# Performance work log

Hardware: AMD Instinct MI355X
Metric: run time of the kernel (lower is better)

The kernel has to match this reference:

```python
import jax, jax.numpy as jnp
import numpy as np

V = 25000
E = 100000
NODE_IN = 74
EDGE_IN = 12
OUT = 64
EHID = 128
NUM_STEPS = 6


def setup_inputs() -> dict:
    key = jax.random.key(0)
    ks = jax.random.split(key, 12)
    s = 0.05
    node_feats = jax.random.normal(ks[0], (V, NODE_IN), dtype=jnp.float32)
    edge_feats = jax.random.normal(ks[1], (E, EDGE_IN), dtype=jnp.float32)
    src = jax.random.randint(ks[2], (E,), 0, V)
    dst = jax.random.randint(ks[3], (E,), 0, V)
    # project_node_feats: Linear(node_in, out)
    Wp = jax.random.normal(ks[4], (NODE_IN, OUT), dtype=jnp.float32) * s
    bp = jnp.zeros((OUT,), dtype=jnp.float32)
    # edge network: Linear(edge_in, ehid) -> ReLU -> Linear(ehid, out*out)
    We1 = jax.random.normal(ks[5], (EDGE_IN, EHID), dtype=jnp.float32) * s
    be1 = jnp.zeros((EHID,), dtype=jnp.float32)
    We2 = jax.random.normal(ks[6], (EHID, OUT * OUT), dtype=jnp.float32) * s
    be2 = jnp.zeros((OUT * OUT,), dtype=jnp.float32)
    # NNConv output bias
    bias = jnp.zeros((OUT,), dtype=jnp.float32)
    return {
        "node_feats": node_feats, "edge_feats": edge_feats,
        "src": src, "dst": dst,
        "Wp": Wp, "bp": bp,
        "We1": We1, "be1": be1, "We2": We2, "be2": be2,
        "bias": bias,
    }


def reference(node_feats, edge_feats, src, dst, Wp, bp, We1, be1, We2, be2, bias):
    # project node features
    h = jax.nn.relu(node_feats @ Wp + bp)  # [V, OUT]
    # per-edge weight matrices (same every step -> hoist out of loop)
    ew = jax.nn.relu(edge_feats @ We1 + be1) @ We2 + be2  # [E, OUT*OUT]
    ew = ew.reshape(E, OUT, OUT)
    for _ in range(NUM_STEPS):
        # gather src node feats, batched matvec, scatter-sum to dst
        msg = jnp.einsum('ei,eio->eo', h[src], ew)  # [E, OUT]
        agg = jax.ops.segment_sum(msg, dst, num_segments=V)  # [V, OUT]
        h = jax.nn.relu(agg + bias)
    return h
```

## Files before the change

kernel.cpp:

```cpp
#include <hip/hip_runtime.h>
#include <hip/hip_bf16.h>

#define Vn 25000
#define En 100000
#define NODE_IN 74
#define EDGE_IN 12
#define OUTD 64
#define EHID 128
#define NUM_STEPS 6

#define HPAD 68

typedef __attribute__((ext_vector_type(8))) _Float16 half8;
typedef __attribute__((ext_vector_type(4))) float floatx4;

__global__ void proj_kernel(const float* __restrict__ node,
                            const float* __restrict__ Wp,
                            const float* __restrict__ bp,
                            float* __restrict__ h) {
  __shared__ float nf[NODE_IN];
  int v = blockIdx.x;
  int o = threadIdx.x;
  for (int i = o; i < NODE_IN; i += 64) nf[i] = node[(size_t)v * NODE_IN + i];
  __syncthreads();
  float acc = bp[o];
  for (int i = 0; i < NODE_IN; ++i) acc = fmaf(nf[i], Wp[i * OUTD + o], acc);
  h[(size_t)v * OUTD + o] = fmaxf(acc, 0.0f);
}

__global__ void edge_kernel(const float* __restrict__ ef,
                            const float* __restrict__ We1,
                            const float* __restrict__ be1,
                            _Float16* __restrict__ f) {
  __shared__ float es[EDGE_IN];
  int e = blockIdx.x;
  int k = threadIdx.x;
  if (k < EDGE_IN) es[k] = ef[(size_t)e * EDGE_IN + k];
  __syncthreads();
  float acc = be1[k];
  for (int j = 0; j < EDGE_IN; ++j) acc = fmaf(es[j], We1[j * EHID + k], acc);
  f[(size_t)e * EHID + k] = (_Float16)fmaxf(acc, 0.0f);
}

__global__ void w2r_kernel(const float* __restrict__ We2,
                           _Float16* __restrict__ w2s) {
  int g = blockIdx.x * 256 + threadIdx.x;
  int j = g & 7;
  int quad = (g >> 3) & 3;
  int l15 = (g >> 5) & 15;
  int c = (g >> 9) & 3;
  int step = g >> 11;
  int s = step & 3;
  int i = step >> 2;
  int k = s * 32 + quad * 8 + j;
  int col = i * 64 + c * 16 + l15;
  int eidx = g & 2047;
  int estore = eidx ^ (((eidx >> 6) & 3) << 3);
  w2s[((size_t)step << 11) | estore] = (_Float16)We2[(size_t)k * (OUTD * OUTD) + col];
}

#define GLOAD_LDS(gp, lp)                                                     \
  __builtin_amdgcn_global_load_lds(                                           \
      (const __attribute__((address_space(1))) void*)(gp),                    \
      (__attribute__((address_space(3))) void*)(lp), 16, 0, 0)

__global__ __launch_bounds__(256, 3) void msg_kernel(
    const float* __restrict__ h,
    const _Float16* __restrict__ f,
    const _Float16* __restrict__ w2s,
    const int* __restrict__ src,
    const int* __restrict__ dst,
    const float* __restrict__ be2,
    float* __restrict__ agg) {
  __shared__ __align__(16) float smem[12544];
  __shared__ int s_dst[64];

  const int tid = threadIdx.x;
  const int wv = tid >> 6;
  const int lane = tid & 63;
  const int quad = lane >> 4;
  const int l15 = lane & 15;
  const int e0 = blockIdx.x * 64;

  if (tid < 64) {
    int e = e0 + tid;
    s_dst[tid] = (e < En) ? dst[e] : -1;
  }
  {
    int e = tid & 63;
    int ib = tid >> 6;
    int eg = e0 + e;
    int sv = (eg < En) ? src[eg] : 0;
    const float4* hp = reinterpret_cast<const float4*>(h + (size_t)sv * OUTD + ib * 16);
    for (int c = 0; c < 4; ++c) {
      float4 val = hp[c];
      int i4 = ib * 16 + c * 4;
      smem[(i4 + 0) * HPAD + e] = val.x;
      smem[(i4 + 1) * HPAD + e] = val.y;
      smem[(i4 + 2) * HPAD + e] = val.z;
      smem[(i4 + 3) * HPAD + e] = val.w;
    }
  }
  __syncthreads();

  half8 afr[4][4];
#pragma unroll
  for (int t = 0; t < 4; ++t) {
    int e = e0 + t * 16 + l15;
    if (e >= En) e = En - 1;
    const _Float16* fr = f + (size_t)e * EHID + quad * 8;
#pragma unroll
    for (int s = 0; s < 4; ++s)
      afr[t][s] = *reinterpret_cast<const half8*>(fr + s * 32);
  }

  floatx4 acc[4][4];
  const floatx4 zero4 = (floatx4){0.f, 0.f, 0.f, 0.f};
#pragma unroll
  for (int t = 0; t < 4; ++t)
#pragma unroll
    for (int c = 0; c < 4; ++c) acc[t][c] = zero4;

  const int ibase = wv * 16;

  char* ring = (char*)smem + 4352 * 4 + wv * 8192;
  const char* w2b = (const char*)w2s;
  const int roff = l15 * 64 + ((quad ^ ((l15 >> 1) & 3)) << 4);
  const char* slot0p = ring + roff;
  const char* slot1p = ring + 4096 + roff;

#define STAGE(GS, SLOT)                                                       \
  {                                                                           \
    const char* gp_ = w2b + (size_t)(GS) * 4096 + lane * 16;                  \
    char* lp_ = ring + (SLOT) * 4096;                                         \
    GLOAD_LDS(gp_, lp_);                                                      \
    GLOAD_LDS(gp_ + 1024, lp_ + 1024);                                        \
    GLOAD_LDS(gp_ + 2048, lp_ + 2048);                                        \
    GLOAD_LDS(gp_ + 3072, lp_ + 3072);                                        \
  }

#define VM4 asm volatile("s_waitcnt vmcnt(4)" ::: "memory")
#define VM0 asm volatile("s_waitcnt vmcnt(0)" ::: "memory")
#define LGKM0 asm volatile("s_waitcnt lgkmcnt(0)" ::: "memory")

#define KSTEP(SS, SLOTP, SLOT, WAIT, DOSTAGE, IV)                             \
  {                                                                           \
    WAIT;                                                                     \
    half8 b0_ = *reinterpret_cast<const half8*>(SLOTP);                       \
    half8 b1_ = *reinterpret_cast<const half8*>(SLOTP + 1024);                \
    half8 b2_ = *reinterpret_cast<const half8*>(SLOTP + 2048);                \
    half8 b3_ = *reinterpret_cast<const half8*>(SLOTP + 3072);                \
    LGKM0;                                                                    \
    __builtin_amdgcn_sched_barrier(0);                                        \
    if (DOSTAGE) STAGE(((IV) << 2) + (SS) + 2, SLOT);                         \
    _Pragma("unroll") for (int t = 0; t < 4; ++t) {                           \
      half8 as = afr[t][SS] * hb[t];                                          \
      acc[t][0] = __builtin_amdgcn_mfma_f32_16x16x32_f16(as, b0_, acc[t][0], 0, 0, 0); \
      acc[t][1] = __builtin_amdgcn_mfma_f32_16x16x32_f16(as, b1_, acc[t][1], 0, 0, 0); \
      acc[t][2] = __builtin_amdgcn_mfma_f32_16x16x32_f16(as, b2_, acc[t][2], 0, 0, 0); \
      acc[t][3] = __builtin_amdgcn_mfma_f32_16x16x32_f16(as, b3_, acc[t][3], 0, 0, 0); \
    }                                                                         \
  }

#define BUILD_HB(IV)                                                          \
  half8 hb[4];                                                                \
  _Pragma("unroll") for (int t = 0; t < 4; ++t) {                             \
    _Float16 hf = (_Float16)smem[(IV) * HPAD + t * 16 + l15];                 \
    hb[t] = (half8){hf, hf, hf, hf, hf, hf, hf, hf};                          \
  }

  STAGE(ibase * 4, 0);
  STAGE(ibase * 4 + 1, 1);

  for (int ii = 0; ii < 15; ++ii) {
    int iv = ibase + ii;
    BUILD_HB(iv);
    KSTEP(0, slot0p, 0, VM4, 1, iv);
    KSTEP(1, slot1p, 1, VM4, 1, iv);
    KSTEP(2, slot0p, 0, VM4, 1, iv);
    KSTEP(3, slot1p, 1, VM4, 1, iv);
  }
  {
    int iv = ibase + 15;
    BUILD_HB(iv);
    KSTEP(0, slot0p, 0, VM4, 1, iv);
    KSTEP(1, slot1p, 1, VM4, 1, iv);
    KSTEP(2, slot0p, 0, VM4, 0, iv);
    KSTEP(3, slot1p, 1, VM0, 0, iv);
  }

  if (wv == 0) {
#pragma unroll
    for (int s = 0; s < 2; ++s) {
      half8 b2f[4];
#pragma unroll
      for (int c = 0; c < 4; ++c) {
        half8 v;
#pragma unroll
        for (int j = 0; j < 8; ++j)
          v[j] = (_Float16)be2[(s * 32 + quad * 8 + j) * 64 + c * 16 + l15];
        b2f[c] = v;
      }
#pragma unroll
      for (int t = 0; t < 4; ++t) {
        half8 ha;
#pragma unroll
        for (int j = 0; j < 8; ++j)
          ha[j] = (_Float16)smem[(s * 32 + quad * 8 + j) * HPAD + t * 16 + l15];
#pragma unroll
        for (int c = 0; c < 4; ++c)
          acc[t][c] = __builtin_amdgcn_mfma_f32_16x16x32_f16(ha, b2f[c], acc[t][c], 0, 0, 0);
      }
    }
  }

  floatx4* scv = reinterpret_cast<floatx4*>(smem);

#define ST1(TG)                                                           \
  _Pragma("unroll") for (int c = 0; c < 4; ++c)                           \
      scv[wv * 512 + (((TG) & 1) * 4 + c) * 64 + lane] = acc[TG][c];
#define LD1(TK)                                                           \
  _Pragma("unroll") for (int c = 0; c < 4; ++c)                           \
      acc[TK][c] += scv[(wv ^ 1) * 512 + (((TK) & 1) * 4 + c) * 64 + lane];
#define ST2(TG)                                                           \
  _Pragma("unroll") for (int c = 0; c < 4; ++c)                           \
      scv[wv * 512 + c * 64 + lane] = acc[TG][c];
#define LD2(TK)                                                           \
  _Pragma("unroll") for (int c = 0; c < 4; ++c)                           \
      acc[TK][c] += scv[(wv ^ 2) * 512 + c * 64 + lane];
#define SCAT(TF)                                                          \
  {                                                                       \
    int rb = (TF) * 16 + quad * 4;                                        \
    _Pragma("unroll") for (int c = 0; c < 4; ++c) {                       \
      int col = c * 16 + l15;                                             \
      _Pragma("unroll") for (int r = 0; r < 4; ++r) {                     \
        int d = s_dst[rb + r];                                            \
        if (d >= 0) atomicAdd(&agg[(size_t)d * OUTD + col], acc[TF][c][r]); \
      }                                                                   \
    }                                                                     \
  }

  __syncthreads();
  if ((wv & 1) == 0) { ST1(2); ST1(3); } else { ST1(0); ST1(1); }
  __syncthreads();
  if ((wv & 1) == 0) { LD1(0); LD1(1); } else { LD1(2); LD1(3); }
  __syncthreads();
  if (wv == 0) { ST2(1); } else if (wv == 1) { ST2(3); }
  else if (wv == 2) { ST2(0); } else { ST2(2); }
  __syncthreads();
  if (wv == 0) { LD2(0); SCAT(0); }
  else if (wv == 1) { LD2(2); SCAT(2); }
  else if (wv == 2) { LD2(1); SCAT(1); }
  else { LD2(3); SCAT(3); }
}

__global__ void update_kernel(float* __restrict__ agg,
                              const float* __restrict__ bias,
                              float* __restrict__ hout,
                              float* __restrict__ dout, int last) {
  int g = blockIdx.x * 256 + threadIdx.x;
  if (g >= Vn * OUTD) return;
  float v = agg[g];
  agg[g] = 0.0f;
  float r = fmaxf(v + bias[g & 63], 0.0f);
  hout[g] = r;
  if (last) dout[g] = r;
}

extern "C" void kernel_launch(void* const* d_in, const int* in_sizes, int n_in,
                              void* d_out, int out_size, void* d_ws, size_t ws_size,
                              hipStream_t stream) {
  const float* node = (const float*)d_in[0];
  const float* edge = (const float*)d_in[1];
  const int* src = (const int*)d_in[2];
  const int* dst = (const int*)d_in[3];
  const float* Wp   = (const float*)d_in[4];
  const float* bp   = (const float*)d_in[5];
  const float* We1  = (const float*)d_in[6];
  const float* be1  = (const float*)d_in[7];
  const float* We2  = (const float*)d_in[8];
  const float* be2  = (const float*)d_in[9];
  const float* bias = (const float*)d_in[10];
  float* out = (float*)d_out;

  char* ws = (char*)d_ws;
  float* agg = (float*)(ws);
  float* h_a = (float*)(ws + 6400000);
  float* h_b = (float*)(ws + 12800000);
  _Float16* f   = (_Float16*)(ws + 19200000);
  _Float16* w2s = (_Float16*)(ws + 44800000);

  hipMemsetAsync(agg, 0, (size_t)Vn * OUTD * sizeof(float), stream);
  proj_kernel<<<Vn, 64, 0, stream>>>(node, Wp, bp, h_a);
  edge_kernel<<<En, 128, 0, stream>>>(edge, We1, be1, f);
  w2r_kernel<<<(OUTD * OUTD * EHID) / 256, 256, 0, stream>>>(We2, w2s);

  float* hin = h_a;
  float* hout = h_b;
  for (int s = 0; s < NUM_STEPS; ++s) {
    msg_kernel<<<(En + 63) / 64, 256, 0, stream>>>(hin, f, w2s, src, dst, be2, agg);
    update_kernel<<<(Vn * OUTD + 255) / 256, 256, 0, stream>>>(
        agg, bias, hout, out, s == NUM_STEPS - 1);
    float* t = hin; hin = hout; hout = t;
  }
}
```

Before: 810.1 us.

## Software-pipeline LDS B-fragment reads with register double buffering in msg kernel

```diff
diff --git a/kernel.cpp b/kernel.cpp
--- a/kernel.cpp
+++ b/kernel.cpp
@@ -64,7 +64,7 @@
       (const __attribute__((address_space(1))) void*)(gp),                    \
       (__attribute__((address_space(3))) void*)(lp), 16, 0, 0)
 
-__global__ __launch_bounds__(256, 3) void msg_kernel(
+__global__ __launch_bounds__(256, 2) void msg_kernel(
     const float* __restrict__ h,
     const _Float16* __restrict__ f,
     const _Float16* __restrict__ w2s,
@@ -72,8 +72,10 @@
     const int* __restrict__ dst,
     const float* __restrict__ be2,
     float* __restrict__ agg) {
-  __shared__ __align__(16) float smem[12544];
+  __shared__ __align__(16) char smem_raw[41472];
   __shared__ int s_dst[64];
+
+  _Float16* h16 = (_Float16*)smem_raw;
 
   const int tid = threadIdx.x;
   const int wv = tid >> 6;
@@ -95,10 +97,10 @@
     for (int c = 0; c < 4; ++c) {
       float4 val = hp[c];
       int i4 = ib * 16 + c * 4;
-      smem[(i4 + 0) * HPAD + e] = val.x;
-      smem[(i4 + 1) * HPAD + e] = val.y;
-      smem[(i4 + 2) * HPAD + e] = val.z;
-      smem[(i4 + 3) * HPAD + e] = val.w;
+      h16[(i4 + 0) * HPAD + e] = (_Float16)val.x;
+      h16[(i4 + 1) * HPAD + e] = (_Float16)val.y;
+      h16[(i4 + 2) * HPAD + e] = (_Float16)val.z;
+      h16[(i4 + 3) * HPAD + e] = (_Float16)val.w;
     }
   }
   __syncthreads();
@@ -123,7 +125,7 @@
 
   const int ibase = wv * 16;
 
-  char* ring = (char*)smem + 4352 * 4 + wv * 8192;
+  char* ring = smem_raw + 8704 + wv * 8192;
   const char* w2b = (const char*)w2s;
   const int roff = l15 * 64 + ((quad ^ ((l15 >> 1) & 3)) << 4);
   const char* slot0p = ring + roff;
@@ -142,51 +144,64 @@
 #define VM4 asm volatile("s_waitcnt vmcnt(4)" ::: "memory")
 #define VM0 asm volatile("s_waitcnt vmcnt(0)" ::: "memory")
 #define LGKM0 asm volatile("s_waitcnt lgkmcnt(0)" ::: "memory")
-
-#define KSTEP(SS, SLOTP, SLOT, WAIT, DOSTAGE, IV)                             \
+#define LGKM4 asm volatile("s_waitcnt lgkmcnt(4)" ::: "memory")
+#define SB __builtin_amdgcn_sched_barrier(0)
+
+#define KSTEP(SS, BCUR, BNXT, STSLOT, GST, LW, VW, DO_STAGE, DO_READ, RDP)    \
   {                                                                           \
-    WAIT;                                                                     \
-    half8 b0_ = *reinterpret_cast<const half8*>(SLOTP);                       \
-    half8 b1_ = *reinterpret_cast<const half8*>(SLOTP + 1024);                \
-    half8 b2_ = *reinterpret_cast<const half8*>(SLOTP + 2048);                \
-    half8 b3_ = *reinterpret_cast<const half8*>(SLOTP + 3072);                \
-    LGKM0;                                                                    \
-    __builtin_amdgcn_sched_barrier(0);                                        \
-    if (DOSTAGE) STAGE(((IV) << 2) + (SS) + 2, SLOT);                         \
+    LW;                                                                       \
+    SB;                                                                       \
+    if (DO_STAGE) STAGE(GST, STSLOT);                                         \
+    VW;                                                                       \
+    if (DO_READ) {                                                            \
+      BNXT[0] = *reinterpret_cast<const half8*>(RDP);                         \
+      BNXT[1] = *reinterpret_cast<const half8*>(RDP + 1024);                  \
+      BNXT[2] = *reinterpret_cast<const half8*>(RDP + 2048);                  \
+      BNXT[3] = *reinterpret_cast<const half8*>(RDP + 3072);                  \
+    }                                                                         \
     _Pragma("unroll") for (int t = 0; t < 4; ++t) {                           \
       half8 as = afr[t][SS] * hb[t];                                          \
-      acc[t][0] = __builtin_amdgcn_mfma_f32_16x16x32_f16(as, b0_, acc[t][0], 0, 0, 0); \
-      acc[t][1] = __builtin_amdgcn_mfma_f32_16x16x32_f16(as, b1_, acc[t][1], 0, 0, 0); \
-      acc[t][2] = __builtin_amdgcn_mfma_f32_16x16x32_f16(as, b2_, acc[t][2], 0, 0, 0); \
-      acc[t][3] = __builtin_amdgcn_mfma_f32_16x16x32_f16(as, b3_, acc[t][3], 0, 0, 0); \
+      acc[t][0] = __builtin_amdgcn_mfma_f32_16x16x32_f16(as, BCUR[0], acc[t][0], 0, 0, 0); \
+      acc[t][1] = __builtin_amdgcn_mfma_f32_16x16x32_f16(as, BCUR[1], acc[t][1], 0, 0, 0); \
+      acc[t][2] = __builtin_amdgcn_mfma_f32_16x16x32_f16(as, BCUR[2], acc[t][2], 0, 0, 0); \
+      acc[t][3] = __builtin_amdgcn_mfma_f32_16x16x32_f16(as, BCUR[3], acc[t][3], 0, 0, 0); \
     }                                                                         \
+    SB;                                                                       \
   }
 
 #define BUILD_HB(IV)                                                          \
   half8 hb[4];                                                                \
   _Pragma("unroll") for (int t = 0; t < 4; ++t) {                             \
-    _Float16 hf = (_Float16)smem[(IV) * HPAD + t * 16 + l15];                 \
+    _Float16 hf = h16[(IV) * HPAD + t * 16 + l15];                            \
     hb[t] = (half8){hf, hf, hf, hf, hf, hf, hf, hf};                          \
   }
 
   STAGE(ibase * 4, 0);
   STAGE(ibase * 4 + 1, 1);
+  VM4;
+  half8 bE[4], bO[4];
+  bE[0] = *reinterpret_cast<const half8*>(slot0p);
+  bE[1] = *reinterpret_cast<const half8*>(slot0p + 1024);
+  bE[2] = *reinterpret_cast<const half8*>(slot0p + 2048);
+  bE[3] = *reinterpret_cast<const half8*>(slot0p + 3072);
 
   for (int ii = 0; ii < 15; ++ii) {
     int iv = ibase + ii;
+    int gs = iv * 4;
     BUILD_HB(iv);
-    KSTEP(0, slot0p, 0, VM4, 1, iv);
-    KSTEP(1, slot1p, 1, VM4, 1, iv);
-    KSTEP(2, slot0p, 0, VM4, 1, iv);
-    KSTEP(3, slot1p, 1, VM4, 1, iv);
+    KSTEP(0, bE, bO, 0, gs + 2, LGKM4, VM4, 1, 1, slot1p);
+    KSTEP(1, bO, bE, 1, gs + 3, LGKM0, VM4, 1, 1, slot0p);
+    KSTEP(2, bE, bO, 0, gs + 4, LGKM0, VM4, 1, 1, slot1p);
+    KSTEP(3, bO, bE, 1, gs + 5, LGKM0, VM4, 1, 1, slot0p);
   }
   {
     int iv = ibase + 15;
+    int gs = iv * 4;
     BUILD_HB(iv);
-    KSTEP(0, slot0p, 0, VM4, 1, iv);
-    KSTEP(1, slot1p, 1, VM4, 1, iv);
-    KSTEP(2, slot0p, 0, VM4, 0, iv);
-    KSTEP(3, slot1p, 1, VM0, 0, iv);
+    KSTEP(0, bE, bO, 0, gs + 2, LGKM4, VM4, 1, 1, slot1p);
+    KSTEP(1, bO, bE, 1, gs + 3, LGKM0, VM4, 1, 1, slot0p);
+    KSTEP(2, bE, bO, 0, 0, LGKM0, VM0, 0, 1, slot1p);
+    KSTEP(3, bO, bE, 1, 0, (void)0, (void)0, 0, 0, slot0p);
   }
 
   if (wv == 0) {
@@ -206,7 +221,7 @@
         half8 ha;
 #pragma unroll
         for (int j = 0; j < 8; ++j)
-          ha[j] = (_Float16)smem[(s * 32 + quad * 8 + j) * HPAD + t * 16 + l15];
+          ha[j] = h16[(s * 32 + quad * 8 + j) * HPAD + t * 16 + l15];
 #pragma unroll
         for (int c = 0; c < 4; ++c)
           acc[t][c] = __builtin_amdgcn_mfma_f32_16x16x32_f16(ha, b2f[c], acc[t][c], 0, 0, 0);
@@ -214,7 +229,7 @@
     }
   }
 
-  floatx4* scv = reinterpret_cast<floatx4*>(smem);
+  floatx4* scv = reinterpret_cast<floatx4*>(smem_raw);
 
 #define ST1(TG)                                                           \
   _Pragma("unroll") for (int c = 0; c < 4; ++c)                           \
```

Result: slower. 839.2 us (+3.6%).

## Run message kernel as single-wave blocks over full K, dropping cross-wave reduction

Applied to the files above, without the earlier changes.

```diff
diff --git a/kernel.cpp b/kernel.cpp
--- a/kernel.cpp
+++ b/kernel.cpp
@@ -8,8 +8,6 @@
 #define OUTD 64
 #define EHID 128
 #define NUM_STEPS 6
-
-#define HPAD 68
 
 typedef __attribute__((ext_vector_type(8))) _Float16 half8;
 typedef __attribute__((ext_vector_type(4))) float floatx4;
@@ -64,7 +62,7 @@
       (const __attribute__((address_space(1))) void*)(gp),                    \
       (__attribute__((address_space(3))) void*)(lp), 16, 0, 0)
 
-__global__ __launch_bounds__(256, 3) void msg_kernel(
+__global__ __launch_bounds__(64, 2) void msg_kernel(
     const float* __restrict__ h,
     const _Float16* __restrict__ f,
     const _Float16* __restrict__ w2s,
@@ -72,36 +70,31 @@
     const int* __restrict__ dst,
     const float* __restrict__ be2,
     float* __restrict__ agg) {
-  __shared__ __align__(16) float smem[12544];
+  __shared__ __align__(16) char smem_raw[16384];
   __shared__ int s_dst[64];
 
-  const int tid = threadIdx.x;
-  const int wv = tid >> 6;
-  const int lane = tid & 63;
+  _Float16* h16 = (_Float16*)smem_raw;
+  char* ring = smem_raw + 8192;
+
+  const int lane = threadIdx.x;
   const int quad = lane >> 4;
   const int l15 = lane & 15;
   const int e0 = blockIdx.x * 64;
 
-  if (tid < 64) {
-    int e = e0 + tid;
-    s_dst[tid] = (e < En) ? dst[e] : -1;
-  }
   {
-    int e = tid & 63;
-    int ib = tid >> 6;
-    int eg = e0 + e;
+    int eg = e0 + lane;
+    s_dst[lane] = (eg < En) ? dst[eg] : -1;
     int sv = (eg < En) ? src[eg] : 0;
-    const float4* hp = reinterpret_cast<const float4*>(h + (size_t)sv * OUTD + ib * 16);
-    for (int c = 0; c < 4; ++c) {
-      float4 val = hp[c];
-      int i4 = ib * 16 + c * 4;
-      smem[(i4 + 0) * HPAD + e] = val.x;
-      smem[(i4 + 1) * HPAD + e] = val.y;
-      smem[(i4 + 2) * HPAD + e] = val.z;
-      smem[(i4 + 3) * HPAD + e] = val.w;
-    }
-  }
-  __syncthreads();
+    const float4* hp = reinterpret_cast<const float4*>(h + (size_t)sv * OUTD);
+#pragma unroll
+    for (int c = 0; c < 16; ++c) {
+      float4 v = hp[c];
+      h16[(c * 4 + 0) * 64 + lane] = (_Float16)v.x;
+      h16[(c * 4 + 1) * 64 + lane] = (_Float16)v.y;
+      h16[(c * 4 + 2) * 64 + lane] = (_Float16)v.z;
+      h16[(c * 4 + 3) * 64 + lane] = (_Float16)v.w;
+    }
+  }
 
   half8 afr[4][4];
 #pragma unroll
@@ -121,13 +114,10 @@
 #pragma unroll
     for (int c = 0; c < 4; ++c) acc[t][c] = zero4;
 
-  const int ibase = wv * 16;
-
-  char* ring = (char*)smem + 4352 * 4 + wv * 8192;
   const char* w2b = (const char*)w2s;
   const int roff = l15 * 64 + ((quad ^ ((l15 >> 1) & 3)) << 4);
-  const char* slot0p = ring + roff;
-  const char* slot1p = ring + 4096 + roff;
+  const char* sp0 = ring + roff;
+  const char* sp1 = ring + 4096 + roff;
 
 #define STAGE(GS, SLOT)                                                       \
   {                                                                           \
@@ -140,56 +130,55 @@
   }
 
 #define VM4 asm volatile("s_waitcnt vmcnt(4)" ::: "memory")
-#define VM0 asm volatile("s_waitcnt vmcnt(0)" ::: "memory")
 #define LGKM0 asm volatile("s_waitcnt lgkmcnt(0)" ::: "memory")
-
-#define KSTEP(SS, SLOTP, SLOT, WAIT, DOSTAGE, IV)                             \
+#define SB __builtin_amdgcn_sched_barrier(0)
+
+#define KSTEP(SS, BMM, BRD, STSLOT, RDP, GST)                                 \
   {                                                                           \
-    WAIT;                                                                     \
-    half8 b0_ = *reinterpret_cast<const half8*>(SLOTP);                       \
-    half8 b1_ = *reinterpret_cast<const half8*>(SLOTP + 1024);                \
-    half8 b2_ = *reinterpret_cast<const half8*>(SLOTP + 2048);                \
-    half8 b3_ = *reinterpret_cast<const half8*>(SLOTP + 3072);                \
     LGKM0;                                                                    \
-    __builtin_amdgcn_sched_barrier(0);                                        \
-    if (DOSTAGE) STAGE(((IV) << 2) + (SS) + 2, SLOT);                         \
+    SB;                                                                       \
+    int gs_ = (GST) > 255 ? 255 : (GST);                                      \
+    STAGE(gs_, STSLOT);                                                       \
+    VM4;                                                                      \
+    BRD[0] = *reinterpret_cast<const half8*>(RDP);                            \
+    BRD[1] = *reinterpret_cast<const half8*>(RDP + 1024);                     \
+    BRD[2] = *reinterpret_cast<const half8*>(RDP + 2048);                     \
+    BRD[3] = *reinterpret_cast<const half8*>(RDP + 3072);                     \
+    __builtin_amdgcn_s_setprio(1);                                            \
     _Pragma("unroll") for (int t = 0; t < 4; ++t) {                           \
       half8 as = afr[t][SS] * hb[t];                                          \
-      acc[t][0] = __builtin_amdgcn_mfma_f32_16x16x32_f16(as, b0_, acc[t][0], 0, 0, 0); \
-      acc[t][1] = __builtin_amdgcn_mfma_f32_16x16x32_f16(as, b1_, acc[t][1], 0, 0, 0); \
-      acc[t][2] = __builtin_amdgcn_mfma_f32_16x16x32_f16(as, b2_, acc[t][2], 0, 0, 0); \
-      acc[t][3] = __builtin_amdgcn_mfma_f32_16x16x32_f16(as, b3_, acc[t][3], 0, 0, 0); \
+      acc[t][0] = __builtin_amdgcn_mfma_f32_16x16x32_f16(as, BMM[0], acc[t][0], 0, 0, 0); \
+      acc[t][1] = __builtin_amdgcn_mfma_f32_16x16x32_f16(as, BMM[1], acc[t][1], 0, 0, 0); \
+      acc[t][2] = __builtin_amdgcn_mfma_f32_16x16x32_f16(as, BMM[2], acc[t][2], 0, 0, 0); \
+      acc[t][3] = __builtin_amdgcn_mfma_f32_16x16x32_f16(as, BMM[3], acc[t][3], 0, 0, 0); \
     }                                                                         \
-  }
-
-#define BUILD_HB(IV)                                                          \
-  half8 hb[4];                                                                \
-  _Pragma("unroll") for (int t = 0; t < 4; ++t) {                             \
-    _Float16 hf = (_Float16)smem[(IV) * HPAD + t * 16 + l15];                 \
-    hb[t] = (half8){hf, hf, hf, hf, hf, hf, hf, hf};                          \
-  }
-
-  STAGE(ibase * 4, 0);
-  STAGE(ibase * 4 + 1, 1);
-
-  for (int ii = 0; ii < 15; ++ii) {
-    int iv = ibase + ii;
-    BUILD_HB(iv);
-    KSTEP(0, slot0p, 0, VM4, 1, iv);
-    KSTEP(1, slot1p, 1, VM4, 1, iv);
-    KSTEP(2, slot0p, 0, VM4, 1, iv);
-    KSTEP(3, slot1p, 1, VM4, 1, iv);
-  }
+    __builtin_amdgcn_s_setprio(0);                                            \
+  }
+
+  STAGE(0, 0);
+  STAGE(1, 1);
+  VM4;
+  half8 P[4], Q[4];
+  P[0] = *reinterpret_cast<const half8*>(sp0);
+  P[1] = *reinterpret_cast<const half8*>(sp0 + 1024);
+  P[2] = *reinterpret_cast<const half8*>(sp0 + 2048);
+  P[3] = *reinterpret_cast<const half8*>(sp0 + 3072);
+
+  for (int i = 0; i < 64; ++i) {
+    half8 hb[4];
+#pragma unroll
+    for (int t = 0; t < 4; ++t) {
+      _Float16 hf = h16[i * 64 + t * 16 + l15];
+      hb[t] = (half8){hf, hf, hf, hf, hf, hf, hf, hf};
+    }
+    int j = i * 4;
+    KSTEP(0, P, Q, 0, sp1, j + 2);
+    KSTEP(1, Q, P, 1, sp0, j + 3);
+    KSTEP(2, P, Q, 0, sp1, j + 4);
+    KSTEP(3, Q, P, 1, sp0, j + 5);
+  }
+
   {
-    int iv = ibase + 15;
-    BUILD_HB(iv);
-    KSTEP(0, slot0p, 0, VM4, 1, iv);
-    KSTEP(1, slot1p, 1, VM4, 1, iv);
-    KSTEP(2, slot0p, 0, VM4, 0, iv);
-    KSTEP(3, slot1p, 1, VM0, 0, iv);
-  }
-
-  if (wv == 0) {
 #pragma unroll
     for (int s = 0; s < 2; ++s) {
       half8 b2f[4];
@@ -206,7 +195,7 @@
         half8 ha;
 #pragma unroll
         for (int j = 0; j < 8; ++j)
-          ha[j] = (_Float16)smem[(s * 32 + quad * 8 + j) * HPAD + t * 16 + l15];
+          ha[j] = h16[(s * 32 + quad * 8 + j) * 64 + t * 16 + l15];
 #pragma unroll
         for (int c = 0; c < 4; ++c)
           acc[t][c] = __builtin_amdgcn_mfma_f32_16x16x32_f16(ha, b2f[c], acc[t][c], 0, 0, 0);
@@ -214,44 +203,19 @@
     }
   }
 
-  floatx4* scv = reinterpret_cast<floatx4*>(smem);
-
-#define ST1(TG)                                                           \
-  _Pragma("unroll") for (int c = 0; c < 4; ++c)                           \
-      scv[wv * 512 + (((TG) & 1) * 4 + c) * 64 + lane] = acc[TG][c];
-#define LD1(TK)                                                           \
-  _Pragma("unroll") for (int c = 0; c < 4; ++c)                           \
-      acc[TK][c] += scv[(wv ^ 1) * 512 + (((TK) & 1) * 4 + c) * 64 + lane];
-#define ST2(TG)                                                           \
-  _Pragma("unroll") for (int c = 0; c < 4; ++c)                           \
-      scv[wv * 512 + c * 64 + lane] = acc[TG][c];
-#define LD2(TK)                                                           \
-  _Pragma("unroll") for (int c = 0; c < 4; ++c)                           \
-      acc[TK][c] += scv[(wv ^ 2) * 512 + c * 64 + lane];
-#define SCAT(TF)                                                          \
-  {                                                                       \
-    int rb = (TF) * 16 + quad * 4;                                        \
-    _Pragma("unroll") for (int c = 0; c < 4; ++c) {                       \
-      int col = c * 16 + l15;                                             \
-      _Pragma("unroll") for (int r = 0; r < 4; ++r) {                     \
-        int d = s_dst[rb + r];                                            \
-        if (d >= 0) atomicAdd(&agg[(size_t)d * OUTD + col], acc[TF][c][r]); \
-      }                                                                   \
-    }                                                                     \
-  }
-
-  __syncthreads();
-  if ((wv & 1) == 0) { ST1(2); ST1(3); } else { ST1(0); ST1(1); }
-  __syncthreads();
-  if ((wv & 1) == 0) { LD1(0); LD1(1); } else { LD1(2); LD1(3); }
-  __syncthreads();
-  if (wv == 0) { ST2(1); } else if (wv == 1) { ST2(3); }
-  else if (wv == 2) { ST2(0); } else { ST2(2); }
-  __syncthreads();
-  if (wv == 0) { LD2(0); SCAT(0); }
-  else if (wv == 1) { LD2(2); SCAT(2); }
-  else if (wv == 2) { LD2(1); SCAT(1); }
-  else { LD2(3); SCAT(3); }
+#pragma unroll
+  for (int t = 0; t < 4; ++t) {
+    int rb = t * 16 + quad * 4;
+#pragma unroll
+    for (int c = 0; c < 4; ++c) {
+      int col = c * 16 + l15;
+#pragma unroll
+      for (int r = 0; r < 4; ++r) {
+        int d = s_dst[rb + r];
+        if (d >= 0) atomicAdd(&agg[(size_t)d * OUTD + col], acc[t][c][r]);
+      }
+    }
+  }
 }
 
 __global__ void update_kernel(float* __restrict__ agg,
@@ -298,7 +262,7 @@
   float* hin = h_a;
   float* hout = h_b;
   for (int s = 0; s < NUM_STEPS; ++s) {
-    msg_kernel<<<(En + 63) / 64, 256, 0, stream>>>(hin, f, w2s, src, dst, be2, agg);
+    msg_kernel<<<(En + 63) / 64, 64, 0, stream>>>(hin, f, w2s, src, dst, be2, agg);
     update_kernel<<<(Vn * OUTD + 255) / 256, 256, 0, stream>>>(
         agg, bias, hout, out, s == NUM_STEPS - 1);
     float* t = hin; hin = hout; hout = t;
```

New measurement: 856.7 us. 1.06x slower.
